# Optimization experiments

Measured on AMD Instinct MI355X. Metric: run time of the kernel, lower is better.

Reference implementation:

```python
import jax, jax.numpy as jnp
import numpy as np

D_MODEL = 1024
N_HEADS = 16
HEAD_DIM = D_MODEL // N_HEADS


def setup_inputs() -> dict:
    key = jax.random.key(0)
    ks = jax.random.split(key, 6)
    B, S = 2, 2048
    scale = 1.0 / np.sqrt(D_MODEL)
    x = jax.random.normal(ks[0], (B, S, D_MODEL), dtype=jnp.float32)
    Wq = jax.random.normal(ks[1], (D_MODEL, D_MODEL), dtype=jnp.float32) * scale
    Wk = jax.random.normal(ks[2], (D_MODEL, D_MODEL), dtype=jnp.float32) * scale
    Wv = jax.random.normal(ks[3], (D_MODEL, D_MODEL), dtype=jnp.float32) * scale
    Wo = jax.random.normal(ks[4], (D_MODEL, D_MODEL), dtype=jnp.float32) * scale
    bo = jax.random.normal(ks[5], (D_MODEL,), dtype=jnp.float32) * 0.02
    return {"x": x, "Wq": Wq, "Wk": Wk, "Wv": Wv, "Wo": Wo, "bo": bo}


def reference(x, Wq, Wk, Wv, Wo, bo):
    B, S, _ = x.shape
    H, hd = N_HEADS, HEAD_DIM
    # qkv projections (no bias, qkv_bias=False)
    q = (x @ Wq).reshape(B, S, H, hd).transpose(0, 2, 1, 3)  # [B,H,S,hd]
    k = (x @ Wk).reshape(B, S, H, hd).transpose(0, 2, 1, 3)
    v = (x @ Wv).reshape(B, S, H, hd).transpose(0, 2, 1, 3)
    scores = jnp.einsum('bhqd,bhkd->bhqk', q, k)  # [B,H,S,S]
    causal = jnp.tril(jnp.ones((S, S), dtype=bool))  # True = keep
    scores = jnp.where(causal, scores, -jnp.inf)
    weights = jax.nn.softmax(scores / np.sqrt(hd), axis=-1)
    # dropout p=0.0 -> identity
    ctx = jnp.einsum('bhqk,bhkd->bhqd', weights, v)  # [B,H,S,hd]
    ctx = ctx.transpose(0, 2, 1, 3).reshape(B, S, H * hd)
    return ctx @ Wo + bo
```

## Files before the change

### kernel.cpp

```cpp
#include <hip/hip_runtime.h>
#include <hip/hip_bf16.h>
#include <stdint.h>

#define SEQ    2048
#define BATCH  2
#define DMODEL 1024
#define NHEADS 16
#define HDIM   64
#define MROWS  (BATCH*SEQ)

typedef __attribute__((ext_vector_type(8))) short bf16x8;
typedef __attribute__((ext_vector_type(4))) short bf16x4;
typedef __attribute__((ext_vector_type(4))) float f32x4;

__device__ inline void global_to_lds16(const void* g, void* l) {
  __builtin_amdgcn_global_load_lds(
      (const __attribute__((address_space(1))) uint32_t*)g,
      (__attribute__((address_space(3))) uint32_t*)l, 16, 0, 0);
}

__device__ inline unsigned short f2bf_bits(float f) {
  __hip_bfloat16 h = __float2bfloat16(f);
  return *(unsigned short*)&h;
}

__global__ void prep_kernel(const float* __restrict__ x, __hip_bfloat16* __restrict__ xb,
                            const float* __restrict__ Wq, const float* __restrict__ Wk,
                            const float* __restrict__ Wv, const float* __restrict__ Wo,
                            __hip_bfloat16* __restrict__ Wqkv_t, __hip_bfloat16* __restrict__ Wo_t) {
  __shared__ float tile[64][69];
  if (blockIdx.x < 1024) {
    int base = (blockIdx.x * 256 + threadIdx.x) * 16;
    short o[16];
#pragma unroll
    for (int j = 0; j < 4; j++) {
      float4 v = *(const float4*)(x + base + j * 4);
      o[j * 4 + 0] = (short)f2bf_bits(v.x);
      o[j * 4 + 1] = (short)f2bf_bits(v.y);
      o[j * 4 + 2] = (short)f2bf_bits(v.z);
      o[j * 4 + 3] = (short)f2bf_bits(v.w);
    }
    *(bf16x8*)(xb + base) = *(const bf16x8*)&o[0];
    *(bf16x8*)(xb + base + 8) = *(const bf16x8*)&o[8];
    return;
  }
  int idx = blockIdx.x - 1024;
  int z = idx >> 8;
  int rem = idx & 255;
  const float* W = (z == 0) ? Wq : (z == 1) ? Wk : (z == 2) ? Wv : Wo;
  __hip_bfloat16* dst = (z < 3) ? (Wqkv_t + (size_t)z * 1024 * 1024) : Wo_t;
  int k0 = (rem & 15) * 64, n0 = (rem >> 4) * 64;
  int ty = threadIdx.x >> 4, tx = threadIdx.x & 15;
#pragma unroll
  for (int r = 0; r < 4; r++) {
    float4 v = *(const float4*)(W + (size_t)(k0 + ty + r * 16) * 1024 + n0 + tx * 4);
    tile[ty + r * 16][tx * 4 + 0] = v.x;
    tile[ty + r * 16][tx * 4 + 1] = v.y;
    tile[ty + r * 16][tx * 4 + 2] = v.z;
    tile[ty + r * 16][tx * 4 + 3] = v.w;
  }
  __syncthreads();
  int sy = threadIdx.x >> 3, sx = threadIdx.x & 7;
#pragma unroll
  for (int s = 0; s < 2; s++) {
    int n = sy + s * 32;
    short u[8];
#pragma unroll
    for (int i = 0; i < 8; i++) u[i] = (short)f2bf_bits(tile[sx * 8 + i][n]);
    *(bf16x8*)(dst + (size_t)(n0 + n) * 1024 + k0 + sx * 8) = *(const bf16x8*)u;
  }
}

template <int TN, bool OUT_BF16, int MINW, bool FUSE_VT>
__global__ __launch_bounds__(256, MINW)
void gemm_kernel(const __hip_bfloat16* __restrict__ A, const __hip_bfloat16* __restrict__ Bt,
                 void* __restrict__ C, const float* __restrict__ bias, int ldc,
                 __hip_bfloat16* __restrict__ Vt) {
  __shared__ __hip_bfloat16 Asl[2][128 * 64];
  __shared__ __hip_bfloat16 Bsl[2][TN * 64];

  const int t = threadIdx.x;
  const int lane = t & 63;
  const int w = t >> 6;
  constexpr int MI = (TN == 128) ? 4 : 2;
  const int wrow = (TN == 128) ? (w >> 1) * 64 : w * 32;
  const int wcol = (TN == 128) ? (w & 1) * 64 : 0;
  const int m0 = blockIdx.y * 128;
  const int n0 = blockIdx.x * TN;

  f32x4 acc[MI][4];
#pragma unroll
  for (int i = 0; i < MI; i++)
#pragma unroll
    for (int j = 0; j < 4; j++) acc[i][j] = (f32x4){0.f, 0.f, 0.f, 0.f};

  const int srow = lane >> 3;
  const int sjc = (lane & 7) ^ srow;
  const int fm = lane & 15;
  const int g4 = lane >> 4;

  auto stage = [&](int k0, int bufi) {
#pragma unroll
    for (int i = 0; i < 4; i++) {
      int seg = i * 4 + w;
      int r = seg * 8 + srow;
      global_to_lds16(A + (size_t)(m0 + r) * 1024 + k0 + sjc * 8,
                      (void*)(&Asl[bufi][0] + seg * 512 + lane * 8));
    }
#pragma unroll
    for (int i = 0; i < TN / 32; i++) {
      int seg = i * 4 + w;
      int r = seg * 8 + srow;
      global_to_lds16(Bt + (size_t)(n0 + r) * 1024 + k0 + sjc * 8,
                      (void*)(&Bsl[bufi][0] + seg * 512 + lane * 8));
    }
  };

  stage(0, 0);
  for (int k0 = 0; k0 < 1024; k0 += 64) {
    const int buf = (k0 >> 6) & 1;
    __syncthreads();

    bf16x8 af[2][MI], bfr[2][4];
#pragma unroll
    for (int kb = 0; kb < 2; kb++) {
#pragma unroll
      for (int mi = 0; mi < MI; mi++) {
        int row = wrow + mi * 16 + fm;
        af[kb][mi] = *(const bf16x8*)(&Asl[buf][0] + row * 64 + (((kb * 4 + g4) ^ (row & 7)) << 3));
      }
#pragma unroll
      for (int ni = 0; ni < 4; ni++) {
        int row = wcol + ni * 16 + fm;
        bfr[kb][ni] = *(const bf16x8*)(&Bsl[buf][0] + row * 64 + (((kb * 4 + g4) ^ (row & 7)) << 3));
      }
    }

    if (k0 + 64 < 1024) stage(k0 + 64, buf ^ 1);

#pragma unroll
    for (int kb = 0; kb < 2; kb++)
#pragma unroll
      for (int mi = 0; mi < MI; mi++)
#pragma unroll
        for (int ni = 0; ni < 4; ni++)
          acc[mi][ni] = __builtin_amdgcn_mfma_f32_16x16x32_bf16(af[kb][mi], bfr[kb][ni], acc[mi][ni], 0, 0, 0);
  }

  const bool vt_block = FUSE_VT && (n0 >= 2048);
#pragma unroll
  for (int mi = 0; mi < MI; mi++) {
    int mb = m0 + wrow + mi * 16 + g4 * 4;
#pragma unroll
    for (int ni = 0; ni < 4; ni++) {
      int n = n0 + wcol + ni * 16 + fm;
      if (vt_block) {
        int nv = n - 2048;
        int bhh = (mb >> 11) * 16 + (nv >> 6);
        int d = nv & 63;
        int s = mb & 2047;
        unsigned short u[4];
#pragma unroll
        for (int r = 0; r < 4; r++) u[r] = f2bf_bits(acc[mi][ni][r]);
        *(ushort4*)(Vt + ((size_t)bhh * 64 + d) * 2048 + s) = *(const ushort4*)u;
      } else {
        float bv = OUT_BF16 ? 0.f : bias[n];
#pragma unroll
        for (int r = 0; r < 4; r++) {
          if (OUT_BF16)
            ((__hip_bfloat16*)C)[(size_t)(mb + r) * ldc + n] = __float2bfloat16(acc[mi][ni][r]);
          else
            ((float*)C)[(size_t)(mb + r) * ldc + n] = acc[mi][ni][r] + bv;
        }
      }
    }
  }
}

__global__ __launch_bounds__(512, 2)
void qkv_gemm_kernel(const __hip_bfloat16* __restrict__ A,
                     const __hip_bfloat16* __restrict__ Bt,
                     __hip_bfloat16* __restrict__ QKV,
                     __hip_bfloat16* __restrict__ Vt) {
  extern __shared__ __align__(128) char smem_raw[];
  __hip_bfloat16* Asl = (__hip_bfloat16*)smem_raw;
  __hip_bfloat16* Bsl = Asl + 2 * 16384;

  const int t = threadIdx.x;
  const int lane = t & 63;
  const int w = t >> 6;
  const int wm = w >> 2;
  const int wn = w & 3;

  const int wgid = blockIdx.y * 12 + blockIdx.x;
  const int swz = (wgid & 7) * 24 + (wgid >> 3);
  const int m0 = (swz / 12) * 256;
  const int n0 = (swz % 12) * 256;

  const int fm = lane & 15;
  const int g4 = lane >> 4;
  const int csrc = (lane & 7) ^ ((lane >> 3) & 7);

  f32x4 acc[8][4];
#pragma unroll
  for (int i = 0; i < 8; i++)
#pragma unroll
    for (int j = 0; j < 4; j++) acc[i][j] = (f32x4){0.f, 0.f, 0.f, 0.f};

  auto stageA = [&](int ktt, int bufi) {
#pragma unroll
    for (int j = 0; j < 4; j++) {
      int seg = w * 4 + j;
      int row = seg * 8 + (lane >> 3);
      global_to_lds16(A + (size_t)(m0 + row) * 1024 + ktt * 64 + csrc * 8,
                      (void*)(Asl + bufi * 16384 + seg * 512 + lane * 8));
    }
  };
  auto stageB = [&](int ktt, int bufi) {
#pragma unroll
    for (int j = 0; j < 4; j++) {
      int seg = w * 4 + j;
      int row = seg * 8 + (lane >> 3);
      global_to_lds16(Bt + (size_t)(n0 + row) * 1024 + ktt * 64 + csrc * 8,
                      (void*)(Bsl + bufi * 16384 + seg * 512 + lane * 8));
    }
  };

  auto load_af = [&](const __hip_bfloat16* Ab, int mi0, int kk, bf16x8 (&af)[4]) {
#pragma unroll
    for (int mi = 0; mi < 4; mi++) {
      int row = wm * 128 + (mi0 + mi) * 16 + fm;
      af[mi] = *(const bf16x8*)(Ab + row * 64 + (((kk * 4 + g4) ^ (fm & 7)) << 3));
    }
  };
  auto load_bf = [&](const __hip_bfloat16* Bb, int kk, bf16x8 (&bf)[4]) {
#pragma unroll
    for (int ni = 0; ni < 4; ni++) {
      int row = wn * 64 + ni * 16 + fm;
      bf[ni] = *(const bf16x8*)(Bb + row * 64 + (((kk * 4 + g4) ^ (fm & 7)) << 3));
    }
  };

  stageA(0, 0); stageB(0, 0);
  asm volatile("s_waitcnt vmcnt(0)" ::: "memory");
  __builtin_amdgcn_s_barrier();

  for (int kt = 0; kt < 16; ++kt) {
    const int buf = kt & 1;
    const __hip_bfloat16* Ab = Asl + buf * 16384;
    const __hip_bfloat16* Bb = Bsl + buf * 16384;
    bf16x8 af[4], bf[4];

    load_af(Ab, 0, 0, af);
    load_bf(Bb, 0, bf);
    if (kt < 15) stageA(kt + 1, buf ^ 1);
    __builtin_amdgcn_s_barrier();
    __builtin_amdgcn_s_setprio(1);
#pragma unroll
    for (int mi = 0; mi < 4; mi++)
#pragma unroll
      for (int ni = 0; ni < 4; ni++)
        acc[mi][ni] = __builtin_amdgcn_mfma_f32_16x16x32_bf16(af[mi], bf[ni], acc[mi][ni], 0, 0, 0);
    __builtin_amdgcn_s_setprio(0);
    __builtin_amdgcn_s_barrier();

    load_af(Ab, 4, 0, af);
    if (kt < 15) stageB(kt + 1, buf ^ 1);
    __builtin_amdgcn_s_barrier();
    __builtin_amdgcn_s_setprio(1);
#pragma unroll
    for (int mi = 0; mi < 4; mi++)
#pragma unroll
      for (int ni = 0; ni < 4; ni++)
        acc[mi + 4][ni] = __builtin_amdgcn_mfma_f32_16x16x32_bf16(af[mi], bf[ni], acc[mi + 4][ni], 0, 0, 0);
    __builtin_amdgcn_s_setprio(0);
    __builtin_amdgcn_s_barrier();

    load_af(Ab, 0, 1, af);
    load_bf(Bb, 1, bf);
    __builtin_amdgcn_s_barrier();
    __builtin_amdgcn_s_setprio(1);
#pragma unroll
    for (int mi = 0; mi < 4; mi++)
#pragma unroll
      for (int ni = 0; ni < 4; ni++)
        acc[mi][ni] = __builtin_amdgcn_mfma_f32_16x16x32_bf16(af[mi], bf[ni], acc[mi][ni], 0, 0, 0);
    __builtin_amdgcn_s_setprio(0);
    __builtin_amdgcn_s_barrier();

    load_af(Ab, 4, 1, af);
    __builtin_amdgcn_s_barrier();
    __builtin_amdgcn_s_setprio(1);
#pragma unroll
    for (int mi = 0; mi < 4; mi++)
#pragma unroll
      for (int ni = 0; ni < 4; ni++)
        acc[mi + 4][ni] = __builtin_amdgcn_mfma_f32_16x16x32_bf16(af[mi], bf[ni], acc[mi + 4][ni], 0, 0, 0);
    __builtin_amdgcn_s_setprio(0);
    asm volatile("s_waitcnt vmcnt(0)" ::: "memory");
    __builtin_amdgcn_s_barrier();
  }

  const bool vt_block = (n0 >= 2048);
#pragma unroll
  for (int mi = 0; mi < 8; mi++) {
    int mb = m0 + wm * 128 + mi * 16 + g4 * 4;
#pragma unroll
    for (int ni = 0; ni < 4; ni++) {
      int n = n0 + wn * 64 + ni * 16 + fm;
      if (vt_block) {
        int nv = n - 2048;
        int bhh = (mb >> 11) * 16 + (nv >> 6);
        int d = nv & 63;
        int ssq = mb & 2047;
        unsigned short u[4];
#pragma unroll
        for (int r = 0; r < 4; r++) u[r] = f2bf_bits(acc[mi][ni][r]);
        *(ushort4*)(Vt + ((size_t)bhh * 64 + d) * 2048 + ssq) = *(const ushort4*)u;
      } else {
#pragma unroll
        for (int r = 0; r < 4; r++)
          QKV[(size_t)(mb + r) * 3072 + n] = __float2bfloat16(acc[mi][ni][r]);
      }
    }
  }
}

__global__ __launch_bounds__(256, 2)
void attn_kernel(const __hip_bfloat16* __restrict__ QKV,
                 const __hip_bfloat16* __restrict__ Vt,
                 __hip_bfloat16* __restrict__ ctx) {
  __shared__ __hip_bfloat16 Klds[2][128 * 64];
  __shared__ __hip_bfloat16 Vlds[2][64 * 128];

  const int t = threadIdx.x;
  const int lane = t & 63;
  const int w = t >> 6;
  const int L = blockIdx.x;
  const int bh = (L & 7) + 8 * ((L >> 3) & 3);
  const int jraw = L >> 5;
  const int jb = (jraw < 8) ? jraw : 23 - jraw;
  const int qtab[2] = { jb, 31 - jb };
  const int b = bh >> 4, h = bh & 15;
  const int fm = lane & 15;
  const int g4 = lane >> 4;
  const int fk = g4 * 8;
  const size_t rowb = (size_t)b * SEQ;
  const float c = 0.18033688011112042f;

  const int krr = lane >> 3;
  const int kjc = (lane & 7) ^ krr;
  const int vrr = lane >> 4;

  bf16x8 qf[2][2];
#pragma unroll
  for (int hh = 0; hh < 2; hh++) {
    const __hip_bfloat16* qp = QKV + (rowb + qtab[hh] * 64 + w * 16 + fm) * 3072 + h * 64 + fk;
    bf16x8 r0 = *(const bf16x8*)qp;
    bf16x8 r1 = *(const bf16x8*)(qp + 32);
#pragma unroll
    for (int i = 0; i < 8; i++) {
      float f0 = __uint_as_float(((unsigned)(unsigned short)r0[i]) << 16) * c;
      float f1 = __uint_as_float(((unsigned)(unsigned short)r1[i]) << 16) * c;
      r0[i] = (short)f2bf_bits(f0);
      r1[i] = (short)f2bf_bits(f1);
    }
    qf[hh][0] = r0; qf[hh][1] = r1;
  }

  bf16x4 ones4;
#pragma unroll
  for (int i = 0; i < 4; i++) ones4[i] = (short)0x3F80;

  f32x4 acc[2][4];
  f32x4 lacc[2];
#pragma unroll
  for (int hh = 0; hh < 2; hh++) {
    lacc[hh] = (f32x4){0.f, 0.f, 0.f, 0.f};
#pragma unroll
    for (int d = 0; d < 4; d++) acc[hh][d] = (f32x4){0.f, 0.f, 0.f, 0.f};
  }

  auto stage = [&](int pt, int bufi) {
    const int kt0 = pt * 128;
#pragma unroll
    for (int i = 0; i < 4; i++) {
      int seg = i * 4 + w;
      int kr = seg * 8 + krr;
      global_to_lds16(QKV + (rowb + kt0 + kr) * 3072 + 1024 + h * 64 + kjc * 8,
                      (void*)(&Klds[bufi][0] + seg * 512 + lane * 8));
      int vd = seg * 4 + vrr;
      int vjc = (lane & 15) ^ ((seg & 1) * 4 + vrr);
      global_to_lds16(Vt + ((size_t)bh * 64 + vd) * 2048 + kt0 + vjc * 8,
                      (void*)(&Vlds[bufi][0] + seg * 512 + lane * 8));
    }
  };

  auto subcompute = [&](const bf16x8 (&kf)[2][4], const bf16x4 (&vf)[4][4], int kts) {
    const bool act0 = (kts <= qtab[0]);
    f32x4 st1[4], st0[4];
#pragma unroll
    for (int ns = 0; ns < 4; ns++) {
      st1[ns] = (f32x4){0.f, 0.f, 0.f, 0.f};
      st0[ns] = (f32x4){0.f, 0.f, 0.f, 0.f};
    }
    __builtin_amdgcn_s_setprio(1);
#pragma unroll
    for (int kk = 0; kk < 2; kk++) {
#pragma unroll
      for (int ns = 0; ns < 4; ns++)
        st1[ns] = __builtin_amdgcn_mfma_f32_16x16x32_bf16(kf[kk][ns], qf[1][kk], st1[ns], 0, 0, 0);
      if (act0)
#pragma unroll
        for (int ns = 0; ns < 4; ns++)
          st0[ns] = __builtin_amdgcn_mfma_f32_16x16x32_bf16(kf[kk][ns], qf[0][kk], st0[ns], 0, 0, 0);
    }
    __builtin_amdgcn_s_setprio(0);
    auto half = [&](const f32x4 (&st)[4], int hh) {
      const bool diag = (kts == qtab[hh]);
#pragma unroll
      for (int ns = 0; ns < 4; ns++) {
        float e[4];
#pragma unroll
        for (int r = 0; r < 4; r++) {
          float p = __builtin_amdgcn_exp2f(st[ns][r]);
          if (diag) {
            int ktl = ns * 16 + g4 * 4 + r;
            p = (ktl > w * 16 + fm) ? 0.f : p;
          }
          e[r] = p;
        }
        unsigned lo = __builtin_amdgcn_perm(__builtin_bit_cast(unsigned, e[1]),
                                            __builtin_bit_cast(unsigned, e[0]), 0x07060302u);
        unsigned hi = __builtin_amdgcn_perm(__builtin_bit_cast(unsigned, e[3]),
                                            __builtin_bit_cast(unsigned, e[2]), 0x07060302u);
        uint2 pp; pp.x = lo; pp.y = hi;
        bf16x4 pf = __builtin_bit_cast(bf16x4, pp);
        __builtin_amdgcn_s_setprio(1);
        lacc[hh] = __builtin_amdgcn_mfma_f32_16x16x16bf16_1k(pf, ones4, lacc[hh], 0, 0, 0);
#pragma unroll
        for (int dd = 0; dd < 4; dd++)
          acc[hh][dd] = __builtin_amdgcn_mfma_f32_16x16x16bf16_1k(pf, vf[dd][ns], acc[hh][dd], 0, 0, 0);
        __builtin_amdgcn_s_setprio(0);
      }
    };
    half(st1, 1);
    if (act0) half(st0, 0);
  };

  auto load_kf = [&](const __hip_bfloat16* Kb, int sc, bf16x8 (&kf)[2][4]) {
#pragma unroll
    for (int kk = 0; kk < 2; kk++)
#pragma unroll
      for (int ns = 0; ns < 4; ns++) {
        int row = sc * 64 + ns * 16 + fm;
        kf[kk][ns] = *(const bf16x8*)(Kb + row * 64 + (((kk * 4 + g4) ^ (fm & 7)) << 3));
      }
  };
  auto load_vf = [&](const __hip_bfloat16* Vb, int sc, bf16x4 (&vf)[4][4]) {
#pragma unroll
    for (int dd = 0; dd < 4; dd++)
#pragma unroll
      for (int ns = 0; ns < 4; ns++) {
        int ch = sc * 8 + ns * 2 + (g4 >> 1);
        vf[dd][ns] = *(const bf16x4*)(Vb + (dd * 16 + fm) * 128 +
                                      ((ch ^ (fm & 7)) << 3) + (g4 & 1) * 4);
      }
  };

  const int lastt = qtab[1];
  const int lastp = lastt >> 1;
  stage(0, 0);
  for (int pt = 0; pt <= lastp; ++pt) {
    __syncthreads();
    const int buf = pt & 1;
    const __hip_bfloat16* Kb = &Klds[buf][0];
    const __hip_bfloat16* Vb = &Vlds[buf][0];

    bf16x8 kf[2][4];
    bf16x4 vf[4][4];
    load_kf(Kb, 0, kf);
    load_vf(Vb, 0, vf);
    if (pt < lastp) stage(pt + 1, buf ^ 1);
    subcompute(kf, vf, pt * 2);

    if (pt * 2 + 1 <= lastt) {
      load_kf(Kb, 1, kf);
      load_vf(Vb, 1, vf);
      subcompute(kf, vf, pt * 2 + 1);
    }
  }

#pragma unroll
  for (int hh = 0; hh < 2; hh++) {
    float rl[4];
#pragma unroll
    for (int r = 0; r < 4; r++) rl[r] = __builtin_amdgcn_rcpf(lacc[hh][r]);
#pragma unroll
    for (int dd = 0; dd < 4; dd++)
#pragma unroll
      for (int r = 0; r < 4; r++) {
        int q = qtab[hh] * 64 + w * 16 + g4 * 4 + r;
        ctx[(rowb + q) * 1024 + h * 64 + dd * 16 + fm] =
            __float2bfloat16(acc[hh][dd][r] * rl[r]);
      }
  }
}

extern "C" void kernel_launch(void* const* d_in, const int* in_sizes, int n_in,
                              void* d_out, int out_size, void* d_ws, size_t ws_size,
                              hipStream_t stream) {
  const float* x  = (const float*)d_in[0];
  const float* Wq = (const float*)d_in[1];
  const float* Wk = (const float*)d_in[2];
  const float* Wv = (const float*)d_in[3];
  const float* Wo = (const float*)d_in[4];
  const float* bo = (const float*)d_in[5];
  float* out = (float*)d_out;

  char* ws = (char*)d_ws;
  __hip_bfloat16* xb     = (__hip_bfloat16*)(ws);
  __hip_bfloat16* Wqkv_t = (__hip_bfloat16*)(ws + (8ull  << 20));
  __hip_bfloat16* Wo_t   = (__hip_bfloat16*)(ws + (14ull << 20));
  __hip_bfloat16* QKV    = (__hip_bfloat16*)(ws + (16ull << 20));
  __hip_bfloat16* ctxb   = (__hip_bfloat16*)(ws + (40ull << 20));
  __hip_bfloat16* Vt     = (__hip_bfloat16*)(ws + (48ull << 20));

  static int qkv_attr_done = 0;
  if (!qkv_attr_done) {
    (void)hipFuncSetAttribute((const void*)qkv_gemm_kernel,
                              hipFuncAttributeMaxDynamicSharedMemorySize, 131072);
    qkv_attr_done = 1;
  }

  prep_kernel<<<dim3(2048), dim3(256), 0, stream>>>(x, xb, Wq, Wk, Wv, Wo, Wqkv_t, Wo_t);
  qkv_gemm_kernel<<<dim3(12, 16), dim3(512), 131072, stream>>>(xb, Wqkv_t, QKV, Vt);
  attn_kernel<<<dim3(512), dim3(256), 0, stream>>>(QKV, Vt, ctxb);
  gemm_kernel<64, false, 2, false><<<dim3(16, 32), dim3(256), 0, stream>>>(
      ctxb, Wo_t, (void*)out, bo, 1024, nullptr);
}
```

Measured before the change: 168.6 us.

## Replace generic output-projection GEMM with dedicated 128x128-tile pipelined kernel

Removes the templated gemm_kernel and adds a specialized oproj_kernel using 128x128 tiles per block (256 blocks) instead of 128x64 (512 blocks). The k-loop splits each 64-wide k step into two halves, with barriers and s_setprio raising priority around the MFMA bursts while the next tile is prefetched into LDS. The goal is more operand reuse per LDS load and better overlap of loads with compute. The cost is fewer blocks for the CU count and more barriers per iteration.

```diff
diff --git a/kernel.cpp b/kernel.cpp
--- a/kernel.cpp
+++ b/kernel.cpp
@@ -71,112 +71,6 @@
   }
 }
 
-template <int TN, bool OUT_BF16, int MINW, bool FUSE_VT>
-__global__ __launch_bounds__(256, MINW)
-void gemm_kernel(const __hip_bfloat16* __restrict__ A, const __hip_bfloat16* __restrict__ Bt,
-                 void* __restrict__ C, const float* __restrict__ bias, int ldc,
-                 __hip_bfloat16* __restrict__ Vt) {
-  __shared__ __hip_bfloat16 Asl[2][128 * 64];
-  __shared__ __hip_bfloat16 Bsl[2][TN * 64];
-
-  const int t = threadIdx.x;
-  const int lane = t & 63;
-  const int w = t >> 6;
-  constexpr int MI = (TN == 128) ? 4 : 2;
-  const int wrow = (TN == 128) ? (w >> 1) * 64 : w * 32;
-  const int wcol = (TN == 128) ? (w & 1) * 64 : 0;
-  const int m0 = blockIdx.y * 128;
-  const int n0 = blockIdx.x * TN;
-
-  f32x4 acc[MI][4];
-#pragma unroll
-  for (int i = 0; i < MI; i++)
-#pragma unroll
-    for (int j = 0; j < 4; j++) acc[i][j] = (f32x4){0.f, 0.f, 0.f, 0.f};
-
-  const int srow = lane >> 3;
-  const int sjc = (lane & 7) ^ srow;
-  const int fm = lane & 15;
-  const int g4 = lane >> 4;
-
-  auto stage = [&](int k0, int bufi) {
-#pragma unroll
-    for (int i = 0; i < 4; i++) {
-      int seg = i * 4 + w;
-      int r = seg * 8 + srow;
-      global_to_lds16(A + (size_t)(m0 + r) * 1024 + k0 + sjc * 8,
-                      (void*)(&Asl[bufi][0] + seg * 512 + lane * 8));
-    }
-#pragma unroll
-    for (int i = 0; i < TN / 32; i++) {
-      int seg = i * 4 + w;
-      int r = seg * 8 + srow;
-      global_to_lds16(Bt + (size_t)(n0 + r) * 1024 + k0 + sjc * 8,
-                      (void*)(&Bsl[bufi][0] + seg * 512 + lane * 8));
-    }
-  };
-
-  stage(0, 0);
-  for (int k0 = 0; k0 < 1024; k0 += 64) {
-    const int buf = (k0 >> 6) & 1;
-    __syncthreads();
-
-    bf16x8 af[2][MI], bfr[2][4];
-#pragma unroll
-    for (int kb = 0; kb < 2; kb++) {
-#pragma unroll
-      for (int mi = 0; mi < MI; mi++) {
-        int row = wrow + mi * 16 + fm;
-        af[kb][mi] = *(const bf16x8*)(&Asl[buf][0] + row * 64 + (((kb * 4 + g4) ^ (row & 7)) << 3));
-      }
-#pragma unroll
-      for (int ni = 0; ni < 4; ni++) {
-        int row = wcol + ni * 16 + fm;
-        bfr[kb][ni] = *(const bf16x8*)(&Bsl[buf][0] + row * 64 + (((kb * 4 + g4) ^ (row & 7)) << 3));
-      }
-    }
-
-    if (k0 + 64 < 1024) stage(k0 + 64, buf ^ 1);
-
-#pragma unroll
-    for (int kb = 0; kb < 2; kb++)
-#pragma unroll
-      for (int mi = 0; mi < MI; mi++)
-#pragma unroll
-        for (int ni = 0; ni < 4; ni++)
-          acc[mi][ni] = __builtin_amdgcn_mfma_f32_16x16x32_bf16(af[kb][mi], bfr[kb][ni], acc[mi][ni], 0, 0, 0);
-  }
-
-  const bool vt_block = FUSE_VT && (n0 >= 2048);
-#pragma unroll
-  for (int mi = 0; mi < MI; mi++) {
-    int mb = m0 + wrow + mi * 16 + g4 * 4;
-#pragma unroll
-    for (int ni = 0; ni < 4; ni++) {
-      int n = n0 + wcol + ni * 16 + fm;
-      if (vt_block) {
-        int nv = n - 2048;
-        int bhh = (mb >> 11) * 16 + (nv >> 6);
-        int d = nv & 63;
-        int s = mb & 2047;
-        unsigned short u[4];
-#pragma unroll
-        for (int r = 0; r < 4; r++) u[r] = f2bf_bits(acc[mi][ni][r]);
-        *(ushort4*)(Vt + ((size_t)bhh * 64 + d) * 2048 + s) = *(const ushort4*)u;
-      } else {
-        float bv = OUT_BF16 ? 0.f : bias[n];
-#pragma unroll
-        for (int r = 0; r < 4; r++) {
-          if (OUT_BF16)
-            ((__hip_bfloat16*)C)[(size_t)(mb + r) * ldc + n] = __float2bfloat16(acc[mi][ni][r]);
-          else
-            ((float*)C)[(size_t)(mb + r) * ldc + n] = acc[mi][ni][r] + bv;
-        }
-      }
-    }
-  }
-}
-
 __global__ __launch_bounds__(512, 2)
 void qkv_gemm_kernel(const __hip_bfloat16* __restrict__ A,
                      const __hip_bfloat16* __restrict__ Bt,
@@ -322,6 +216,119 @@
         for (int r = 0; r < 4; r++)
           QKV[(size_t)(mb + r) * 3072 + n] = __float2bfloat16(acc[mi][ni][r]);
       }
+    }
+  }
+}
+
+__global__ __launch_bounds__(256, 2)
+void oproj_kernel(const __hip_bfloat16* __restrict__ A,
+                  const __hip_bfloat16* __restrict__ Bt,
+                  float* __restrict__ C,
+                  const float* __restrict__ bias) {
+  __shared__ __hip_bfloat16 Asl[2][128 * 64];
+  __shared__ __hip_bfloat16 Bsl[2][128 * 64];
+
+  const int t = threadIdx.x;
+  const int lane = t & 63;
+  const int w = t >> 6;
+  const int wm = w >> 1;
+  const int wn = w & 1;
+
+  const int wgid = blockIdx.y * 8 + blockIdx.x;
+  const int n0 = (wgid & 7) * 128;
+  const int m0 = (wgid >> 3) * 128;
+
+  const int fm = lane & 15;
+  const int g4 = lane >> 4;
+  const int csrc = (lane & 7) ^ ((lane >> 3) & 7);
+
+  f32x4 acc[4][4];
+#pragma unroll
+  for (int i = 0; i < 4; i++)
+#pragma unroll
+    for (int j = 0; j < 4; j++) acc[i][j] = (f32x4){0.f, 0.f, 0.f, 0.f};
+
+  auto stageA = [&](int ktt, int bufi) {
+#pragma unroll
+    for (int j = 0; j < 4; j++) {
+      int seg = w * 4 + j;
+      int row = seg * 8 + (lane >> 3);
+      global_to_lds16(A + (size_t)(m0 + row) * 1024 + ktt * 64 + csrc * 8,
+                      (void*)(&Asl[bufi][0] + seg * 512 + lane * 8));
+    }
+  };
+  auto stageB = [&](int ktt, int bufi) {
+#pragma unroll
+    for (int j = 0; j < 4; j++) {
+      int seg = w * 4 + j;
+      int row = seg * 8 + (lane >> 3);
+      global_to_lds16(Bt + (size_t)(n0 + row) * 1024 + ktt * 64 + csrc * 8,
+                      (void*)(&Bsl[bufi][0] + seg * 512 + lane * 8));
+    }
+  };
+
+  auto load_af = [&](const __hip_bfloat16* Ab, int kk, bf16x8 (&af)[4]) {
+#pragma unroll
+    for (int mi = 0; mi < 4; mi++) {
+      int row = wm * 64 + mi * 16 + fm;
+      af[mi] = *(const bf16x8*)(Ab + row * 64 + (((kk * 4 + g4) ^ (fm & 7)) << 3));
+    }
+  };
+  auto load_bf = [&](const __hip_bfloat16* Bb, int kk, bf16x8 (&bf)[4]) {
+#pragma unroll
+    for (int ni = 0; ni < 4; ni++) {
+      int row = wn * 64 + ni * 16 + fm;
+      bf[ni] = *(const bf16x8*)(Bb + row * 64 + (((kk * 4 + g4) ^ (fm & 7)) << 3));
+    }
+  };
+
+  stageA(0, 0); stageB(0, 0);
+  asm volatile("s_waitcnt vmcnt(0)" ::: "memory");
+  __builtin_amdgcn_s_barrier();
+
+  for (int kt = 0; kt < 16; ++kt) {
+    const int buf = kt & 1;
+    const __hip_bfloat16* Ab = &Asl[buf][0];
+    const __hip_bfloat16* Bb = &Bsl[buf][0];
+    bf16x8 af[4], bf[4];
+
+    load_af(Ab, 0, af);
+    load_bf(Bb, 0, bf);
+    if (kt < 15) { stageA(kt + 1, buf ^ 1); stageB(kt + 1, buf ^ 1); }
+    __builtin_amdgcn_s_barrier();
+    __builtin_amdgcn_s_setprio(1);
+#pragma unroll
+    for (int mi = 0; mi < 4; mi++)
+#pragma unroll
+      for (int ni = 0; ni < 4; ni++)
+        acc[mi][ni] = __builtin_amdgcn_mfma_f32_16x16x32_bf16(af[mi], bf[ni], acc[mi][ni], 0, 0, 0);
+    __builtin_amdgcn_s_setprio(0);
+    __builtin_amdgcn_s_barrier();
+
+    load_af(Ab, 1, af);
+    load_bf(Bb, 1, bf);
+    __builtin_amdgcn_s_barrier();
+    __builtin_amdgcn_s_setprio(1);
+#pragma unroll
+    for (int mi = 0; mi < 4; mi++)
+#pragma unroll
+      for (int ni = 0; ni < 4; ni++)
+        acc[mi][ni] = __builtin_amdgcn_mfma_f32_16x16x32_bf16(af[mi], bf[ni], acc[mi][ni], 0, 0, 0);
+    __builtin_amdgcn_s_setprio(0);
+    asm volatile("s_waitcnt vmcnt(0)" ::: "memory");
+    __builtin_amdgcn_s_barrier();
+  }
+
+#pragma unroll
+  for (int mi = 0; mi < 4; mi++) {
+    int mb = m0 + wm * 64 + mi * 16 + g4 * 4;
+#pragma unroll
+    for (int ni = 0; ni < 4; ni++) {
+      int n = n0 + wn * 64 + ni * 16 + fm;
+      float bv = bias[n];
+#pragma unroll
+      for (int r = 0; r < 4; r++)
+        C[(size_t)(mb + r) * 1024 + n] = acc[mi][ni][r] + bv;
     }
   }
 }
@@ -536,6 +543,5 @@
   prep_kernel<<<dim3(2048), dim3(256), 0, stream>>>(x, xb, Wq, Wk, Wv, Wo, Wqkv_t, Wo_t);
   qkv_gemm_kernel<<<dim3(12, 16), dim3(512), 131072, stream>>>(xb, Wqkv_t, QKV, Vt);
   attn_kernel<<<dim3(512), dim3(256), 0, stream>>>(QKV, Vt, ctxb);
-  gemm_kernel<64, false, 2, false><<<dim3(16, 32), dim3(256), 0, stream>>>(
-      ctxb, Wo_t, (void*)out, bo, 1024, nullptr);
-}
+  oproj_kernel<<<dim3(8, 32), dim3(256), 0, stream>>>(ctxb, Wo_t, out, bo);
+}
```

Result: no change. 170.4 us (+1.1%).
